# Optimization experiments

Measured on AMD Instinct MI355X. Metric: run time of the kernel, lower is better.

The kernel has to match this reference:

```python
import jax, jax.numpy as jnp
import numpy as np

EMB = 1024
HEADS = 16
DK = EMB // HEADS
EPS = 1e-5


def setup_inputs() -> dict:
    key = jax.random.key(0)
    ks = jax.random.split(key, 7)
    s_in = 1.0 / np.sqrt(EMB)
    return {
        "x": jax.random.normal(ks[0], (4, 2048, EMB), dtype=jnp.float32),
        "W_qkv": jax.random.uniform(ks[1], (EMB, 3 * EMB), jnp.float32, -s_in, s_in),
        "b_qkv": jax.random.uniform(ks[2], (3 * EMB,), jnp.float32, -s_in, s_in),
        "W_out": jax.random.uniform(ks[3], (EMB, EMB), jnp.float32, -s_in, s_in),
        "b_out": jax.random.uniform(ks[4], (EMB,), jnp.float32, -s_in, s_in),
        "gamma": jnp.ones((EMB,), jnp.float32),
        "beta": jnp.zeros((EMB,), jnp.float32),
    }


def reference(x, W_qkv, b_qkv, W_out, b_out, gamma, beta):
    B, T, D = x.shape
    qkv = x @ W_qkv + b_qkv                      # [B,T,3D]
    q, k, v = jnp.split(qkv, 3, axis=-1)
    # [B,T,D] -> [B,H,T,dk]
    def heads(t):
        return t.reshape(B, T, HEADS, DK).transpose(0, 2, 1, 3)
    q, k, v = heads(q), heads(k), heads(v)
    scores = jnp.einsum("bhtd,bhsd->bhts", q, k) / np.sqrt(DK)
    attn = jax.nn.softmax(scores, axis=-1)
    out = jnp.einsum("bhts,bhsd->bhtd", attn, v)  # [B,H,T,dk]
    out = out.transpose(0, 2, 1, 3).reshape(B, T, D)
    out = out @ W_out + b_out
    res = x + out
    mu = jnp.mean(res, axis=-1, keepdims=True)
    var = jnp.mean((res - mu) ** 2, axis=-1, keepdims=True)
    return (res - mu) / jnp.sqrt(var + EPS) * gamma + beta
```

## Files before the change

kernel.cpp:

```cpp
#include <hip/hip_runtime.h>

#define B_ 4
#define T_ 2048
#define D_ 1024
#define H_ 16
#define DK_ 64
#define M_ (B_*T_)

typedef __bf16 bf16;
typedef __bf16 bf16x8 __attribute__((ext_vector_type(8)));
typedef __bf16 bf16x4 __attribute__((ext_vector_type(4)));
typedef short s16x4 __attribute__((ext_vector_type(4)));
typedef float f32x4 __attribute__((ext_vector_type(4)));

__device__ __forceinline__ f32x4 zero4() { f32x4 v = {0.f, 0.f, 0.f, 0.f}; return v; }

__device__ __forceinline__ float fexp2(float x) {
  float r;
  asm("v_exp_f32 %0, %1\n\ts_nop 0" : "=v"(r) : "v"(x));
  return r;
}

__device__ __forceinline__ float max3f(float a, float b, float c) {
  float r;
  asm("v_max3_f32 %0, %1, %2, %3" : "=v"(r) : "v"(a), "v"(b), "v"(c));
  return r;
}

__device__ __forceinline__ void g2l16(const void* g, void* l) {
  __builtin_amdgcn_global_load_lds(
      (const __attribute__((address_space(1))) void*)g,
      (__attribute__((address_space(3))) void*)l, 16, 0, 0);
}

__global__ __launch_bounds__(256) void cast_bf16(const float* __restrict__ src,
                                                 bf16* __restrict__ dst) {
  const size_t i = ((size_t)blockIdx.x * 256 + threadIdx.x) * 8;
  float4 a = *(const float4*)(src + i);
  float4 b = *(const float4*)(src + i + 4);
  bf16x8 v;
  v[0] = (bf16)a.x; v[1] = (bf16)a.y; v[2] = (bf16)a.z; v[3] = (bf16)a.w;
  v[4] = (bf16)b.x; v[5] = (bf16)b.y; v[6] = (bf16)b.z; v[7] = (bf16)b.w;
  *(bf16x8*)(dst + i) = v;
}

__global__ __launch_bounds__(256) void transpose_wf(const float* __restrict__ src,
                                                    bf16* __restrict__ dst, int R, int C) {
  __shared__ alignas(16) bf16 ts[64 * 65];
  const int tid = threadIdx.x;
  const int r0 = blockIdx.x * 64, c0 = blockIdx.y * 64;
  {
    int rr = tid >> 2, cc = (tid & 3) * 16;
    const float4* p4 = (const float4*)(src + (size_t)(r0 + rr) * C + c0 + cc);
    float fv[16];
#pragma unroll
    for (int q = 0; q < 4; ++q) *(float4*)&fv[q * 4] = p4[q];
#pragma unroll
    for (int i = 0; i < 16; ++i) ts[(cc + i) * 65 + rr] = (bf16)fv[i];
  }
  __syncthreads();
  {
    int rr = tid >> 2, cc = (tid & 3) * 16;
    bf16x8 a, b;
#pragma unroll
    for (int i = 0; i < 8; ++i) a[i] = ts[rr * 65 + cc + i];
#pragma unroll
    for (int i = 0; i < 8; ++i) b[i] = ts[rr * 65 + cc + 8 + i];
    bf16* q = dst + (size_t)(c0 + rr) * R + r0 + cc;
    *(bf16x8*)q = a;
    *(bf16x8*)(q + 8) = b;
  }
}

__global__ __launch_bounds__(256) void transpose_v(const bf16* __restrict__ qkv,
                                                   bf16* __restrict__ Vt) {
  __shared__ alignas(16) bf16 ts[64 * 65];
  int bid = blockIdx.x;
  const int tt = bid & 31; bid >>= 5;
  const int h = bid & 15;  const int b = bid >> 4;
  const int t0 = tt * 64;
  const int tid = threadIdx.x;
  {
    int tok = tid >> 2, fc = (tid & 3) * 16;
    const bf16* p = qkv + (size_t)(b * T_ + t0 + tok) * (3 * D_) + 2 * D_ + h * DK_ + fc;
    bf16x8 a = *(const bf16x8*)p;
    bf16x8 c = *(const bf16x8*)(p + 8);
#pragma unroll
    for (int i = 0; i < 8; ++i) ts[(fc + i) * 65 + tok] = a[i];
#pragma unroll
    for (int i = 0; i < 8; ++i) ts[(fc + 8 + i) * 65 + tok] = c[i];
  }
  __syncthreads();
  {
    int f = tid >> 2, tc = (tid & 3) * 16;
    bf16x8 a, c;
#pragma unroll
    for (int i = 0; i < 8; ++i) a[i] = ts[f * 65 + tc + i];
#pragma unroll
    for (int i = 0; i < 8; ++i) c[i] = ts[f * 65 + tc + 8 + i];
    bf16* q = Vt + ((size_t)(b * H_ + h) * DK_ + f) * T_ + t0 + tc;
    *(bf16x8*)q = a;
    *(bf16x8*)(q + 8) = c;
  }
}

template <int ASRC, bool FUSE>
__global__ __launch_bounds__(256) void gemm128(const void* __restrict__ Av,
                                               const bf16* __restrict__ Bt,
                                               const float* __restrict__ bias,
                                               bf16* __restrict__ Cbf,
                                               float* __restrict__ Cf,
                                               const float* __restrict__ resid,
                                               int N, int K, int lda, int ldc) {
  __shared__ alignas(16) bf16 As[128 * 32];
  __shared__ alignas(16) bf16 Bs[128 * 32];
  const int tid = threadIdx.x;
  const int wid = tid >> 6, lane = tid & 63, quad = lane >> 4, l16 = lane & 15;
  const int m0 = blockIdx.x * 128, n0 = blockIdx.y * 128;
  const int wr = (wid >> 1) * 64, wc = (wid & 1) * 64;

  f32x4 acc[4][4];
#pragma unroll
  for (int i = 0; i < 4; ++i)
#pragma unroll
    for (int j = 0; j < 4; ++j) acc[i][j] = zero4();

  for (int k0 = 0; k0 < K; k0 += 32) {
    bf16x8 ar[2];
    if (ASRC == 0) {
#pragma unroll
      for (int p = 0; p < 2; ++p) {
        int t = p * 256 + tid;
        int row = t >> 2, kc = (t & 3) * 8;
        const float* ap = (const float*)Av + (size_t)(m0 + row) * lda + k0 + kc;
        float4 a0 = *(const float4*)ap, a1 = *(const float4*)(ap + 4);
        bf16x8 v;
        v[0] = (bf16)a0.x; v[1] = (bf16)a0.y; v[2] = (bf16)a0.z; v[3] = (bf16)a0.w;
        v[4] = (bf16)a1.x; v[5] = (bf16)a1.y; v[6] = (bf16)a1.z; v[7] = (bf16)a1.w;
        ar[p] = v;
      }
    }
    __syncthreads();
#pragma unroll
    for (int p = 0; p < 2; ++p) {
      int t = p * 256 + tid;
      int row = t >> 2, kc = (t & 3) * 8;
      g2l16(Bt + (size_t)(n0 + row) * K + k0 + kc, (char*)Bs + p * 4096 + wid * 1024);
      if (ASRC == 1)
        g2l16((const bf16*)Av + (size_t)(m0 + row) * lda + k0 + kc,
              (char*)As + p * 4096 + wid * 1024);
      else
        *(bf16x8*)&As[row * 32 + kc] = ar[p];
    }
    __syncthreads();
    bf16x8 af[4], bfr[4];
#pragma unroll
    for (int i = 0; i < 4; ++i)
      af[i] = *(const bf16x8*)&As[(wr + i * 16 + l16) * 32 + quad * 8];
#pragma unroll
    for (int j = 0; j < 4; ++j)
      bfr[j] = *(const bf16x8*)&Bs[(wc + j * 16 + l16) * 32 + quad * 8];
#pragma unroll
    for (int i = 0; i < 4; ++i)
#pragma unroll
      for (int j = 0; j < 4; ++j)
        acc[i][j] = __builtin_amdgcn_mfma_f32_16x16x32_bf16(af[i], bfr[j], acc[i][j], 0, 0, 0);
  }

#pragma unroll
  for (int i = 0; i < 4; ++i) {
#pragma unroll
    for (int j = 0; j < 4; ++j) {
      const int col = n0 + wc + j * 16 + l16;
      const float bv = bias[col];
#pragma unroll
      for (int r = 0; r < 4; ++r) {
        const int row = m0 + wr + i * 16 + quad * 4 + r;
        const float v = acc[i][j][r] + bv;
        if (FUSE) {
          const size_t off = (size_t)row * N + col;
          Cf[off] = v + resid[off];
        } else {
          Cbf[(size_t)row * ldc + col] = (bf16)v;
        }
      }
    }
  }
}

__global__ __launch_bounds__(512) void attn128(const bf16* __restrict__ qkv,
                                               const bf16* __restrict__ Vt,
                                               bf16* __restrict__ out) {
  __shared__ alignas(16) bf16 Ks[128 * 72];
  __shared__ alignas(16) bf16 Vs[64 * 136];
  const int tid = threadIdx.x;
  const int wid = tid >> 6, lane = tid & 63, quad = lane >> 4, l16 = lane & 15;
  const int bid = blockIdx.x;
  const int qb = bid & 15, h = (bid >> 4) & 15, b = bid >> 8;
  const int q0 = qb * 128;

  const int skey = tid >> 3, sf = (tid & 7) * 8;
  const int svf = tid >> 4, skc = (tid & 15) * 8;
  const bf16* kbase = qkv + (size_t)(b * T_ + skey) * (3 * D_) + D_ + h * DK_ + sf;
  const bf16* vbase = Vt + ((size_t)(b * H_ + h) * DK_ + svf) * T_ + skc;

  const float SC = 0.125f * 1.44269504f;
  bf16x8 qf[2];
  {
    const bf16* qp = qkv + (size_t)(b * T_ + q0 + wid * 16 + l16) * (3 * D_) + h * DK_ + quad * 8;
    qf[0] = *(const bf16x8*)qp;
    qf[1] = *(const bf16x8*)(qp + 32);
#pragma unroll
    for (int i = 0; i < 8; ++i) { qf[0][i] = (bf16)((float)qf[0][i] * SC);
                                  qf[1][i] = (bf16)((float)qf[1][i] * SC); }
  }

  float mi = -1e30f, li = 0.f;
  f32x4 o[4];
#pragma unroll
  for (int ft = 0; ft < 4; ++ft) o[ft] = zero4();

  bf16x8 kr[2], vr[2];
#pragma unroll
  for (int p = 0; p < 2; ++p) {
    kr[p] = *(const bf16x8*)(kbase + (size_t)(p * 64) * (3 * D_));
    vr[p] = *(const bf16x8*)(vbase + (size_t)(p * 32) * T_);
  }

  for (int kt = 0; kt < T_ / 128; ++kt) {
    __syncthreads();
#pragma unroll
    for (int p = 0; p < 2; ++p) {
      *(bf16x8*)&Ks[(skey + p * 64) * 72 + sf] = kr[p];
      *(bf16x8*)&Vs[(svf + p * 32) * 136 + skc] = vr[p];
    }
    __syncthreads();
    if (kt + 1 < T_ / 128) {
      const size_t koff = (size_t)(kt + 1) * 128;
#pragma unroll
      for (int p = 0; p < 2; ++p) {
        kr[p] = *(const bf16x8*)(kbase + (koff + p * 64) * (3 * D_));
        vr[p] = *(const bf16x8*)(vbase + (size_t)(p * 32) * T_ + koff);
      }
    }

    f32x4 sv[8];
#pragma unroll
    for (int nt = 0; nt < 8; ++nt) sv[nt] = zero4();
    __builtin_amdgcn_s_setprio(1);
#pragma unroll
    for (int nt = 0; nt < 8; ++nt)
#pragma unroll
      for (int ks = 0; ks < 2; ++ks) {
        bf16x8 kf = *(const bf16x8*)&Ks[(nt * 16 + l16) * 72 + ks * 32 + quad * 8];
        sv[nt] = __builtin_amdgcn_mfma_f32_16x16x32_bf16(kf, qf[ks], sv[nt], 0, 0, 0);
      }
    __builtin_amdgcn_s_setprio(0);

    float t0 = max3f(sv[0][0], sv[0][1], sv[0][2]);
    float t1 = max3f(sv[0][3], sv[1][0], sv[1][1]);
    t0 = max3f(t0, sv[1][2], sv[1][3]);
#pragma unroll
    for (int nt = 2; nt < 8; nt += 2) {
      t0 = max3f(t0, sv[nt][0], sv[nt][1]);
      t1 = max3f(t1, sv[nt][2], sv[nt][3]);
      t0 = max3f(t0, sv[nt + 1][0], sv[nt + 1][1]);
      t1 = max3f(t1, sv[nt + 1][2], sv[nt + 1][3]);
    }
    float tmax = fmaxf(t0, t1);
    tmax = fmaxf(tmax, __shfl_xor(tmax, 16, 64));
    tmax = fmaxf(tmax, __shfl_xor(tmax, 32, 64));

    if (!__all(tmax <= mi + 8.f)) {
      const float nm = fmaxf(mi, tmax);
      const float alpha = fexp2(mi - nm);
      mi = nm;
      li *= alpha;
#pragma unroll
      for (int r = 0; r < 4; ++r) {
        const float ar = __shfl(alpha, quad * 4 + r, 64);
#pragma unroll
        for (int ft = 0; ft < 4; ++ft) o[ft][r] *= ar;
      }
    }

    f32x4 s4 = zero4();
#pragma unroll
    for (int nt = 0; nt < 8; ++nt) {
      f32x4 d = sv[nt] - mi;
      d[0] = fexp2(d[0]); d[1] = fexp2(d[1]); d[2] = fexp2(d[2]); d[3] = fexp2(d[3]);
      sv[nt] = d;
      s4 += d;
    }
    float s = (s4[0] + s4[1]) + (s4[2] + s4[3]);
    s += __shfl_xor(s, 16, 64);
    s += __shfl_xor(s, 32, 64);
    li += s;

    __builtin_amdgcn_s_setprio(1);
#pragma unroll
    for (int ks = 0; ks < 8; ++ks) {
      union { bf16x4 b; s16x4 s; } pf;
#pragma unroll
      for (int j = 0; j < 4; ++j) pf.b[j] = (bf16)sv[ks][j];
#pragma unroll
      for (int ft = 0; ft < 4; ++ft) {
        const s16x4 vf = *(const s16x4*)&Vs[(ft * 16 + l16) * 136 + ks * 16 + quad * 4];
        o[ft] = __builtin_amdgcn_mfma_f32_16x16x16bf16_1k(pf.s, vf, o[ft], 0, 0, 0);
      }
    }
    __builtin_amdgcn_s_setprio(0);
  }

#pragma unroll
  for (int r = 0; r < 4; ++r) {
    const float inv = 1.0f / __shfl(li, quad * 4 + r, 64);
    const int row = b * T_ + q0 + wid * 16 + quad * 4 + r;
#pragma unroll
    for (int ft = 0; ft < 4; ++ft)
      out[(size_t)row * (3 * D_) + h * DK_ + ft * 16 + l16] = (bf16)(o[ft][r] * inv);
  }
}

__global__ __launch_bounds__(256) void ln_out(float* __restrict__ res,
                                              const float* __restrict__ gamma,
                                              const float* __restrict__ beta) {
  const int row = blockIdx.x * 4 + (threadIdx.x >> 6);
  const int lane = threadIdx.x & 63;
  float4 v[4];
  float s = 0.f, q = 0.f;
#pragma unroll
  for (int p = 0; p < 4; ++p) {
    v[p] = *(const float4*)(res + (size_t)row * D_ + p * 256 + lane * 4);
    s += v[p].x + v[p].y + v[p].z + v[p].w;
    q += v[p].x * v[p].x + v[p].y * v[p].y + v[p].z * v[p].z + v[p].w * v[p].w;
  }
#pragma unroll
  for (int m = 1; m < 64; m <<= 1) { s += __shfl_xor(s, m, 64); q += __shfl_xor(q, m, 64); }
  const float mu = s * (1.0f / D_);
  const float var = q * (1.0f / D_) - mu * mu;
  const float rstd = rsqrtf(var + 1e-5f);
#pragma unroll
  for (int p = 0; p < 4; ++p) {
    const int c = p * 256 + lane * 4;
    const float4 g = *(const float4*)(gamma + c);
    const float4 be = *(const float4*)(beta + c);
    float4 ov;
    ov.x = (v[p].x - mu) * rstd * g.x + be.x;
    ov.y = (v[p].y - mu) * rstd * g.y + be.y;
    ov.z = (v[p].z - mu) * rstd * g.z + be.z;
    ov.w = (v[p].w - mu) * rstd * g.w + be.w;
    *(float4*)(res + (size_t)row * D_ + c) = ov;
  }
}

extern "C" void kernel_launch(void* const* d_in, const int* in_sizes, int n_in,
                              void* d_out, int out_size, void* d_ws, size_t ws_size,
                              hipStream_t stream) {
  const float* x     = (const float*)d_in[0];
  const float* Wqkv  = (const float*)d_in[1];
  const float* bqkv  = (const float*)d_in[2];
  const float* Wout  = (const float*)d_in[3];
  const float* bout  = (const float*)d_in[4];
  const float* gamma = (const float*)d_in[5];
  const float* beta  = (const float*)d_in[6];
  float* out = (float*)d_out;

  char* ws = (char*)d_ws;
  bf16* WqkvT = (bf16*)ws; ws += (size_t)3 * D_ * D_ * 2;
  bf16* WoutT = (bf16*)ws; ws += (size_t)D_ * D_ * 2;
  bf16* qkv   = (bf16*)ws; ws += (size_t)M_ * 3 * D_ * 2;
  bf16* Vt    = (bf16*)ws;
  bf16* attn  = qkv + 2 * D_;
  bf16* xb    = Vt;

  transpose_wf<<<dim3(D_ / 64, 3 * D_ / 64), 256, 0, stream>>>(Wqkv, WqkvT, D_, 3 * D_);
  transpose_wf<<<dim3(D_ / 64, D_ / 64), 256, 0, stream>>>(Wout, WoutT, D_, D_);
  cast_bf16<<<M_ * D_ / (256 * 8), 256, 0, stream>>>(x, xb);
  gemm128<1, false><<<dim3(M_ / 128, 3 * D_ / 128), 256, 0, stream>>>(
      xb, WqkvT, bqkv, qkv, nullptr, nullptr, 3 * D_, D_, D_, 3 * D_);
  transpose_v<<<B_ * H_ * (T_ / 64), 256, 0, stream>>>(qkv, Vt);
  attn128<<<B_ * H_ * (T_ / 128), 512, 0, stream>>>(qkv, Vt, attn);
  gemm128<1, true><<<dim3(M_ / 128, D_ / 128), 256, 0, stream>>>(
      attn, WoutT, bout, nullptr, out, x, D_, D_, 3 * D_, D_);
  ln_out<<<M_ / 4, 256, 0, stream>>>(out, gamma, beta);
}
```

Measured before the change: 336.2 us.

## Process two 16-row query tiles per wave in attention to reuse K/V tiles

After: 333.2 us. About the same (-0.9%).

```diff
diff --git a/kernel.cpp b/kernel.cpp
--- a/kernel.cpp
+++ b/kernel.cpp
@@ -188,16 +188,16 @@
   }
 }
 
-__global__ __launch_bounds__(512) void attn128(const bf16* __restrict__ qkv,
-                                               const bf16* __restrict__ Vt,
-                                               bf16* __restrict__ out) {
+__global__ __launch_bounds__(512, 2) void attn256(const bf16* __restrict__ qkv,
+                                                  const bf16* __restrict__ Vt,
+                                                  bf16* __restrict__ out) {
   __shared__ alignas(16) bf16 Ks[128 * 72];
   __shared__ alignas(16) bf16 Vs[64 * 136];
   const int tid = threadIdx.x;
   const int wid = tid >> 6, lane = tid & 63, quad = lane >> 4, l16 = lane & 15;
   const int bid = blockIdx.x;
-  const int qb = bid & 15, h = (bid >> 4) & 15, b = bid >> 8;
-  const int q0 = qb * 128;
+  const int qb = bid & 7, h = (bid >> 3) & 15, b = bid >> 7;
+  const int q0 = qb * 256;
 
   const int skey = tid >> 3, sf = (tid & 7) * 8;
   const int svf = tid >> 4, skc = (tid & 15) * 8;
@@ -205,20 +205,23 @@
   const bf16* vbase = Vt + ((size_t)(b * H_ + h) * DK_ + svf) * T_ + skc;
 
   const float SC = 0.125f * 1.44269504f;
-  bf16x8 qf[2];
+  bf16x8 qA[2], qB[2];
   {
-    const bf16* qp = qkv + (size_t)(b * T_ + q0 + wid * 16 + l16) * (3 * D_) + h * DK_ + quad * 8;
-    qf[0] = *(const bf16x8*)qp;
-    qf[1] = *(const bf16x8*)(qp + 32);
-#pragma unroll
-    for (int i = 0; i < 8; ++i) { qf[0][i] = (bf16)((float)qf[0][i] * SC);
-                                  qf[1][i] = (bf16)((float)qf[1][i] * SC); }
-  }
-
-  float mi = -1e30f, li = 0.f;
-  f32x4 o[4];
-#pragma unroll
-  for (int ft = 0; ft < 4; ++ft) o[ft] = zero4();
+    const bf16* qpA = qkv + (size_t)(b * T_ + q0 + wid * 32 + l16) * (3 * D_) + h * DK_ + quad * 8;
+    const bf16* qpB = qpA + (size_t)16 * (3 * D_);
+    qA[0] = *(const bf16x8*)qpA;       qA[1] = *(const bf16x8*)(qpA + 32);
+    qB[0] = *(const bf16x8*)qpB;       qB[1] = *(const bf16x8*)(qpB + 32);
+#pragma unroll
+    for (int i = 0; i < 8; ++i) {
+      qA[0][i] = (bf16)((float)qA[0][i] * SC); qA[1][i] = (bf16)((float)qA[1][i] * SC);
+      qB[0][i] = (bf16)((float)qB[0][i] * SC); qB[1][i] = (bf16)((float)qB[1][i] * SC);
+    }
+  }
+
+  float miA = -1e30f, liA = 0.f, miB = -1e30f, liB = 0.f;
+  f32x4 oA[4], oB[4];
+#pragma unroll
+  for (int ft = 0; ft < 4; ++ft) { oA[ft] = zero4(); oB[ft] = zero4(); }
 
   bf16x8 kr[2], vr[2];
 #pragma unroll
@@ -244,81 +247,116 @@
       }
     }
 
-    f32x4 sv[8];
-#pragma unroll
-    for (int nt = 0; nt < 8; ++nt) sv[nt] = zero4();
+    f32x4 svA[8], svB[8];
+#pragma unroll
+    for (int nt = 0; nt < 8; ++nt) { svA[nt] = zero4(); svB[nt] = zero4(); }
     __builtin_amdgcn_s_setprio(1);
 #pragma unroll
     for (int nt = 0; nt < 8; ++nt)
 #pragma unroll
       for (int ks = 0; ks < 2; ++ks) {
         bf16x8 kf = *(const bf16x8*)&Ks[(nt * 16 + l16) * 72 + ks * 32 + quad * 8];
-        sv[nt] = __builtin_amdgcn_mfma_f32_16x16x32_bf16(kf, qf[ks], sv[nt], 0, 0, 0);
+        svA[nt] = __builtin_amdgcn_mfma_f32_16x16x32_bf16(kf, qA[ks], svA[nt], 0, 0, 0);
+        svB[nt] = __builtin_amdgcn_mfma_f32_16x16x32_bf16(kf, qB[ks], svB[nt], 0, 0, 0);
       }
     __builtin_amdgcn_s_setprio(0);
 
-    float t0 = max3f(sv[0][0], sv[0][1], sv[0][2]);
-    float t1 = max3f(sv[0][3], sv[1][0], sv[1][1]);
-    t0 = max3f(t0, sv[1][2], sv[1][3]);
+    float a0 = max3f(svA[0][0], svA[0][1], svA[0][2]);
+    float a1 = max3f(svA[0][3], svA[1][0], svA[1][1]);
+    a0 = max3f(a0, svA[1][2], svA[1][3]);
+    float b0 = max3f(svB[0][0], svB[0][1], svB[0][2]);
+    float b1 = max3f(svB[0][3], svB[1][0], svB[1][1]);
+    b0 = max3f(b0, svB[1][2], svB[1][3]);
 #pragma unroll
     for (int nt = 2; nt < 8; nt += 2) {
-      t0 = max3f(t0, sv[nt][0], sv[nt][1]);
-      t1 = max3f(t1, sv[nt][2], sv[nt][3]);
-      t0 = max3f(t0, sv[nt + 1][0], sv[nt + 1][1]);
-      t1 = max3f(t1, sv[nt + 1][2], sv[nt + 1][3]);
-    }
-    float tmax = fmaxf(t0, t1);
-    tmax = fmaxf(tmax, __shfl_xor(tmax, 16, 64));
-    tmax = fmaxf(tmax, __shfl_xor(tmax, 32, 64));
-
-    if (!__all(tmax <= mi + 8.f)) {
-      const float nm = fmaxf(mi, tmax);
-      const float alpha = fexp2(mi - nm);
-      mi = nm;
-      li *= alpha;
+      a0 = max3f(a0, svA[nt][0], svA[nt][1]);
+      a1 = max3f(a1, svA[nt][2], svA[nt][3]);
+      a0 = max3f(a0, svA[nt + 1][0], svA[nt + 1][1]);
+      a1 = max3f(a1, svA[nt + 1][2], svA[nt + 1][3]);
+      b0 = max3f(b0, svB[nt][0], svB[nt][1]);
+      b1 = max3f(b1, svB[nt][2], svB[nt][3]);
+      b0 = max3f(b0, svB[nt + 1][0], svB[nt + 1][1]);
+      b1 = max3f(b1, svB[nt + 1][2], svB[nt + 1][3]);
+    }
+    float tA = fmaxf(a0, a1), tB = fmaxf(b0, b1);
+    tA = fmaxf(tA, __shfl_xor(tA, 16, 64));
+    tA = fmaxf(tA, __shfl_xor(tA, 32, 64));
+    tB = fmaxf(tB, __shfl_xor(tB, 16, 64));
+    tB = fmaxf(tB, __shfl_xor(tB, 32, 64));
+
+    if (!__all(tA <= miA + 8.f)) {
+      const float nm = fmaxf(miA, tA);
+      const float al = fexp2(miA - nm);
+      miA = nm; liA *= al;
 #pragma unroll
       for (int r = 0; r < 4; ++r) {
-        const float ar = __shfl(alpha, quad * 4 + r, 64);
-#pragma unroll
-        for (int ft = 0; ft < 4; ++ft) o[ft][r] *= ar;
-      }
-    }
-
-    f32x4 s4 = zero4();
+        const float ar = __shfl(al, quad * 4 + r, 64);
+#pragma unroll
+        for (int ft = 0; ft < 4; ++ft) oA[ft][r] *= ar;
+      }
+    }
+    if (!__all(tB <= miB + 8.f)) {
+      const float nm = fmaxf(miB, tB);
+      const float al = fexp2(miB - nm);
+      miB = nm; liB *= al;
+#pragma unroll
+      for (int r = 0; r < 4; ++r) {
+        const float ar = __shfl(al, quad * 4 + r, 64);
+#pragma unroll
+        for (int ft = 0; ft < 4; ++ft) oB[ft][r] *= ar;
+      }
+    }
+
+    s16x4 pA[8], pB[8];
+    f32x4 s4A = zero4(), s4B = zero4();
 #pragma unroll
     for (int nt = 0; nt < 8; ++nt) {
-      f32x4 d = sv[nt] - mi;
-      d[0] = fexp2(d[0]); d[1] = fexp2(d[1]); d[2] = fexp2(d[2]); d[3] = fexp2(d[3]);
-      sv[nt] = d;
-      s4 += d;
-    }
-    float s = (s4[0] + s4[1]) + (s4[2] + s4[3]);
-    s += __shfl_xor(s, 16, 64);
-    s += __shfl_xor(s, 32, 64);
-    li += s;
+      f32x4 dA = svA[nt] - miA;
+      dA[0] = fexp2(dA[0]); dA[1] = fexp2(dA[1]); dA[2] = fexp2(dA[2]); dA[3] = fexp2(dA[3]);
+      s4A += dA;
+      union { bf16x4 b; s16x4 s; } ua;
+#pragma unroll
+      for (int j = 0; j < 4; ++j) ua.b[j] = (bf16)dA[j];
+      pA[nt] = ua.s;
+      f32x4 dB = svB[nt] - miB;
+      dB[0] = fexp2(dB[0]); dB[1] = fexp2(dB[1]); dB[2] = fexp2(dB[2]); dB[3] = fexp2(dB[3]);
+      s4B += dB;
+      union { bf16x4 b; s16x4 s; } ub;
+#pragma unroll
+      for (int j = 0; j < 4; ++j) ub.b[j] = (bf16)dB[j];
+      pB[nt] = ub.s;
+    }
+    float sA = (s4A[0] + s4A[1]) + (s4A[2] + s4A[3]);
+    float sB = (s4B[0] + s4B[1]) + (s4B[2] + s4B[3]);
+    sA += __shfl_xor(sA, 16, 64);
+    sA += __shfl_xor(sA, 32, 64);
+    sB += __shfl_xor(sB, 16, 64);
+    sB += __shfl_xor(sB, 32, 64);
+    liA += sA; liB += sB;
 
     __builtin_amdgcn_s_setprio(1);
 #pragma unroll
-    for (int ks = 0; ks < 8; ++ks) {
-      union { bf16x4 b; s16x4 s; } pf;
-#pragma unroll
-      for (int j = 0; j < 4; ++j) pf.b[j] = (bf16)sv[ks][j];
+    for (int ks = 0; ks < 8; ++ks)
 #pragma unroll
       for (int ft = 0; ft < 4; ++ft) {
         const s16x4 vf = *(const s16x4*)&Vs[(ft * 16 + l16) * 136 + ks * 16 + quad * 4];
-        o[ft] = __builtin_amdgcn_mfma_f32_16x16x16bf16_1k(pf.s, vf, o[ft], 0, 0, 0);
-      }
-    }
+        oA[ft] = __builtin_amdgcn_mfma_f32_16x16x16bf16_1k(pA[ks], vf, oA[ft], 0, 0, 0);
+        oB[ft] = __builtin_amdgcn_mfma_f32_16x16x16bf16_1k(pB[ks], vf, oB[ft], 0, 0, 0);
+      }
     __builtin_amdgcn_s_setprio(0);
   }
 
 #pragma unroll
   for (int r = 0; r < 4; ++r) {
-    const float inv = 1.0f / __shfl(li, quad * 4 + r, 64);
-    const int row = b * T_ + q0 + wid * 16 + quad * 4 + r;
-#pragma unroll
-    for (int ft = 0; ft < 4; ++ft)
-      out[(size_t)row * (3 * D_) + h * DK_ + ft * 16 + l16] = (bf16)(o[ft][r] * inv);
+    const float invA = 1.0f / __shfl(liA, quad * 4 + r, 64);
+    const float invB = 1.0f / __shfl(liB, quad * 4 + r, 64);
+    const int rowA = b * T_ + q0 + wid * 32 + quad * 4 + r;
+    const int rowB = rowA + 16;
+#pragma unroll
+    for (int ft = 0; ft < 4; ++ft) {
+      out[(size_t)rowA * (3 * D_) + h * DK_ + ft * 16 + l16] = (bf16)(oA[ft][r] * invA);
+      out[(size_t)rowB * (3 * D_) + h * DK_ + ft * 16 + l16] = (bf16)(oB[ft][r] * invB);
+    }
   }
 }
 
@@ -380,7 +418,7 @@
   gemm128<1, false><<<dim3(M_ / 128, 3 * D_ / 128), 256, 0, stream>>>(
       xb, WqkvT, bqkv, qkv, nullptr, nullptr, 3 * D_, D_, D_, 3 * D_);
   transpose_v<<<B_ * H_ * (T_ / 64), 256, 0, stream>>>(qkv, Vt);
-  attn128<<<B_ * H_ * (T_ / 128), 512, 0, stream>>>(qkv, Vt, attn);
+  attn256<<<B_ * H_ * (T_ / 256), 512, 0, stream>>>(qkv, Vt, attn);
   gemm128<1, true><<<dim3(M_ / 128, D_ / 128), 256, 0, stream>>>(
       attn, WoutT, bout, nullptr, out, x, D_, D_, 3 * D_, D_);
   ln_out<<<M_ / 4, 256, 0, stream>>>(out, gamma, beta);
```
